# Kernel tuning notes

Hardware: AMD Instinct MI355X
Metric: run time of the kernel (lower is better)

## Reference

```python
import jax, jax.numpy as jnp
import numpy as np

I = 2          # input_features
M = 2          # num_membership_functions
R = M * M      # rules (pairs (m,n) for inputs 0 and 1)
N = 4_194_304  # batch size


def setup_inputs() -> dict:
    key = jax.random.key(0)
    k_x, k_w, k_b = jax.random.split(key, 3)
    x = jax.random.normal(k_x, (I, N), dtype=jnp.float32)
    # generalized-bell MF params from membership_funcs_params [[a,b,c]...]
    a = jnp.ones((I, M), dtype=jnp.float32)                      # widths
    b = jnp.full((I, M), 2.0, dtype=jnp.float32)                 # slopes
    c = jnp.tile(jnp.array([-1.0, 1.0], dtype=jnp.float32), (I, 1))  # centers
    # per-rule first-order Sugeno (TSK) defuzzifier: f_r = W[r] . x + Bd[r]
    W = 0.1 * jax.random.normal(k_w, (R, I), dtype=jnp.float32)
    Bd = 0.1 * jax.random.normal(k_b, (R,), dtype=jnp.float32)
    return {"x": x, "a": a, "b": b, "c": c, "W": W, "Bd": Bd}


def reference(x, a, b, c, W, Bd):
    # Layer 1+2 (fuzzification): generalized bell mu = 1/(1+|(x-c)/a|^(2b))
    # mu: [I, M, N]
    mu = 1.0 / (1.0 + jnp.abs((x[:, None, :] - c[:, :, None]) / a[:, :, None]) ** (2.0 * b[:, :, None]))
    # Layer 3 (rule firing strengths): product over the (i=0,m)x(j=1,n) pairs
    # rule index r = m*M + n, matching the original nested loop order. [R, N]
    rules = (mu[0, :, None, :] * mu[1, None, :, :]).reshape(R, N)
    # Layer 4 (normalization): w_r / sum_r w_r
    norm = rules / jnp.sum(rules, axis=0, keepdims=True)
    # Layer 5 (defuzzification): per-rule linear consequent, weighted
    f = W @ x + Bd[:, None]            # [R, N]
    # Layer 6 (aggregation): sum over rules -> [N]
    return jnp.sum(norm * f, axis=0)
```

## Files before the change

### kernel.cpp

```cpp
#include <hip/hip_runtime.h>


__global__ __launch_bounds__(256) void anfis_kernel(
    const float* __restrict__ x,
    const float* __restrict__ a,
    const float* __restrict__ b,
    const float* __restrict__ c,
    const float* __restrict__ W,
    const float* __restrict__ Bd,
    float* __restrict__ out,
    int N)
{
    float ia[2][2], nca[2][2], tb[2][2];
#pragma unroll
    for (int i = 0; i < 2; ++i) {
#pragma unroll
        for (int m = 0; m < 2; ++m) {
            float av = a[i * 2 + m];
            float bv = b[i * 2 + m];
            float cv = c[i * 2 + m];
            float r  = 1.0f / av;
            ia[i][m]  = r;
            nca[i][m] = -cv * r;
            tb[i][m]  = 2.0f * bv;
        }
    }
    float w0[4], w1[4], bd[4];
#pragma unroll
    for (int r = 0; r < 4; ++r) {
        w0[r] = W[r * 2 + 0];
        w1[r] = W[r * 2 + 1];
        bd[r] = Bd[r];
    }

    int idx = (blockIdx.x * blockDim.x + threadIdx.x) * 4;
    if (idx >= N) return;

    float4 v0 = *reinterpret_cast<const float4*>(x + idx);
    float4 v1 = *reinterpret_cast<const float4*>(x + N + idx);

    float xs0[4] = {v0.x, v0.y, v0.z, v0.w};
    float xs1[4] = {v1.x, v1.y, v1.z, v1.w};
    float res[4];

#pragma unroll
    for (int k = 0; k < 4; ++k) {
        float x0 = xs0[k], x1 = xs1[k];

        float mu0[2], mu1[2];
#pragma unroll
        for (int m = 0; m < 2; ++m) {
            float t = fabsf(fmaf(x0, ia[0][m], nca[0][m]));
            float u = __builtin_amdgcn_exp2f(tb[0][m] * __builtin_amdgcn_logf(t));
            mu0[m] = __builtin_amdgcn_rcpf(1.0f + u);
            float s = fabsf(fmaf(x1, ia[1][m], nca[1][m]));
            float v = __builtin_amdgcn_exp2f(tb[1][m] * __builtin_amdgcn_logf(s));
            mu1[m] = __builtin_amdgcn_rcpf(1.0f + v);
        }

        float den = (mu0[0] + mu0[1]) * (mu1[0] + mu1[1]);

        float num = 0.0f;
#pragma unroll
        for (int m = 0; m < 2; ++m) {
#pragma unroll
            for (int n2 = 0; n2 < 2; ++n2) {
                int r = m * 2 + n2;
                float f = fmaf(w0[r], x0, fmaf(w1[r], x1, bd[r]));
                num = fmaf(mu0[m] * mu1[n2], f, num);
            }
        }
        res[k] = num * __builtin_amdgcn_rcpf(den);
    }

    float4 o = {res[0], res[1], res[2], res[3]};
    *reinterpret_cast<float4*>(out + idx) = o;
}

extern "C" void kernel_launch(void* const* d_in, const int* in_sizes, int n_in,
                              void* d_out, int out_size, void* d_ws, size_t ws_size,
                              hipStream_t stream) {
    const float* x  = (const float*)d_in[0];
    const float* a  = (const float*)d_in[1];
    const float* b  = (const float*)d_in[2];
    const float* c  = (const float*)d_in[3];
    const float* W  = (const float*)d_in[4];
    const float* Bd = (const float*)d_in[5];
    float* out = (float*)d_out;

    int N = out_size;
    int n4 = (N + 3) / 4;
    int block = 256;
    int grid = (n4 + block - 1) / block;

    anfis_kernel<<<grid, block, 0, stream>>>(x, a, b, c, W, Bd, out, N);
}
```

Measured before the change: 16.27 us.

## Specialize bell MF for b=2 with polynomial eval and drop per-MF reciprocals

Rewrites the normalization algebraically, multiplying numerator and denominator by the product of the (1+u) terms. This removes the four reciprocals per element. It adds a runtime-checked fast path for b==2, where |x|^4 is computed by squaring instead of log/exp2; the general path stays as a fallback. It also processes 8 elements per thread with two float4 loads and stores per input. The kernel is largely bandwidth bound, so the ALU savings may only partly show, and the larger per-thread work changes the grid size.

```diff
diff --git a/kernel.cpp b/kernel.cpp
--- a/kernel.cpp
+++ b/kernel.cpp
@@ -12,6 +12,7 @@
     int N)
 {
     float ia[2][2], nca[2][2], tb[2][2];
+    bool all_b2 = true;
 #pragma unroll
     for (int i = 0; i < 2; ++i) {
 #pragma unroll
@@ -23,6 +24,7 @@
             ia[i][m]  = r;
             nca[i][m] = -cv * r;
             tb[i][m]  = 2.0f * bv;
+            all_b2 = all_b2 && (bv == 2.0f);
         }
     }
     float w0[4], w1[4], bd[4];
@@ -33,48 +35,72 @@
         bd[r] = Bd[r];
     }
 
-    int idx = (blockIdx.x * blockDim.x + threadIdx.x) * 4;
+    int idx = (blockIdx.x * blockDim.x + threadIdx.x) * 8;
     if (idx >= N) return;
 
-    float4 v0 = *reinterpret_cast<const float4*>(x + idx);
-    float4 v1 = *reinterpret_cast<const float4*>(x + N + idx);
+    const float4* p0 = reinterpret_cast<const float4*>(x + idx);
+    const float4* p1 = reinterpret_cast<const float4*>(x + N + idx);
+    float4 v0a = p0[0], v0b = p0[1];
+    float4 v1a = p1[0], v1b = p1[1];
 
-    float xs0[4] = {v0.x, v0.y, v0.z, v0.w};
-    float xs1[4] = {v1.x, v1.y, v1.z, v1.w};
-    float res[4];
+    float xs0[8] = {v0a.x, v0a.y, v0a.z, v0a.w, v0b.x, v0b.y, v0b.z, v0b.w};
+    float xs1[8] = {v1a.x, v1a.y, v1a.z, v1a.w, v1b.x, v1b.y, v1b.z, v1b.w};
+    float res[8];
 
+    if (all_b2) {
 #pragma unroll
-    for (int k = 0; k < 4; ++k) {
-        float x0 = xs0[k], x1 = xs1[k];
+        for (int k = 0; k < 8; ++k) {
+            float x0 = xs0[k], x1 = xs1[k];
+            float t00 = fmaf(x0, ia[0][0], nca[0][0]); t00 *= t00;
+            float t01 = fmaf(x0, ia[0][1], nca[0][1]); t01 *= t01;
+            float t10 = fmaf(x1, ia[1][0], nca[1][0]); t10 *= t10;
+            float t11 = fmaf(x1, ia[1][1], nca[1][1]); t11 *= t11;
+            float A0 = fmaf(t00, t00, 1.0f);
+            float A1 = fmaf(t01, t01, 1.0f);
+            float B0 = fmaf(t10, t10, 1.0f);
+            float B1 = fmaf(t11, t11, 1.0f);
 
-        float mu0[2], mu1[2];
+            float den = (A0 + A1) * (B0 + B1);
+
+            float f0 = fmaf(w0[0], x0, fmaf(w1[0], x1, bd[0]));
+            float f1 = fmaf(w0[1], x0, fmaf(w1[1], x1, bd[1]));
+            float f2 = fmaf(w0[2], x0, fmaf(w1[2], x1, bd[2]));
+            float f3 = fmaf(w0[3], x0, fmaf(w1[3], x1, bd[3]));
+            float num = (A1 * B1) * f0;
+            num = fmaf(A1 * B0, f1, num);
+            num = fmaf(A0 * B1, f2, num);
+            num = fmaf(A0 * B0, f3, num);
+
+            res[k] = num * __builtin_amdgcn_rcpf(den);
+        }
+    } else {
 #pragma unroll
-        for (int m = 0; m < 2; ++m) {
-            float t = fabsf(fmaf(x0, ia[0][m], nca[0][m]));
-            float u = __builtin_amdgcn_exp2f(tb[0][m] * __builtin_amdgcn_logf(t));
-            mu0[m] = __builtin_amdgcn_rcpf(1.0f + u);
-            float s = fabsf(fmaf(x1, ia[1][m], nca[1][m]));
-            float v = __builtin_amdgcn_exp2f(tb[1][m] * __builtin_amdgcn_logf(s));
-            mu1[m] = __builtin_amdgcn_rcpf(1.0f + v);
+        for (int k = 0; k < 8; ++k) {
+            float x0 = xs0[k], x1 = xs1[k];
+            float u00 = __builtin_amdgcn_exp2f(tb[0][0] * __builtin_amdgcn_logf(fabsf(fmaf(x0, ia[0][0], nca[0][0]))));
+            float u01 = __builtin_amdgcn_exp2f(tb[0][1] * __builtin_amdgcn_logf(fabsf(fmaf(x0, ia[0][1], nca[0][1]))));
+            float u10 = __builtin_amdgcn_exp2f(tb[1][0] * __builtin_amdgcn_logf(fabsf(fmaf(x1, ia[1][0], nca[1][0]))));
+            float u11 = __builtin_amdgcn_exp2f(tb[1][1] * __builtin_amdgcn_logf(fabsf(fmaf(x1, ia[1][1], nca[1][1]))));
+            float A0 = 1.0f + u00, A1 = 1.0f + u01;
+            float B0 = 1.0f + u10, B1 = 1.0f + u11;
+            float den = (A0 + A1) * (B0 + B1);
+            float f0 = fmaf(w0[0], x0, fmaf(w1[0], x1, bd[0]));
+            float f1 = fmaf(w0[1], x0, fmaf(w1[1], x1, bd[1]));
+            float f2 = fmaf(w0[2], x0, fmaf(w1[2], x1, bd[2]));
+            float f3 = fmaf(w0[3], x0, fmaf(w1[3], x1, bd[3]));
+            float num = (A1 * B1) * f0;
+            num = fmaf(A1 * B0, f1, num);
+            num = fmaf(A0 * B1, f2, num);
+            num = fmaf(A0 * B0, f3, num);
+            res[k] = num * __builtin_amdgcn_rcpf(den);
         }
-
-        float den = (mu0[0] + mu0[1]) * (mu1[0] + mu1[1]);
-
-        float num = 0.0f;
-#pragma unroll
-        for (int m = 0; m < 2; ++m) {
-#pragma unroll
-            for (int n2 = 0; n2 < 2; ++n2) {
-                int r = m * 2 + n2;
-                float f = fmaf(w0[r], x0, fmaf(w1[r], x1, bd[r]));
-                num = fmaf(mu0[m] * mu1[n2], f, num);
-            }
-        }
-        res[k] = num * __builtin_amdgcn_rcpf(den);
     }
 
-    float4 o = {res[0], res[1], res[2], res[3]};
-    *reinterpret_cast<float4*>(out + idx) = o;
+    float4 oA = {res[0], res[1], res[2], res[3]};
+    float4 oB = {res[4], res[5], res[6], res[7]};
+    float4* po = reinterpret_cast<float4*>(out + idx);
+    po[0] = oA;
+    po[1] = oB;
 }
 
 extern "C" void kernel_launch(void* const* d_in, const int* in_sizes, int n_in,
@@ -89,9 +115,9 @@
     float* out = (float*)d_out;
 
     int N = out_size;
-    int n4 = (N + 3) / 4;
+    int n8 = (N + 7) / 8;
     int block = 256;
-    int grid = (n4 + block - 1) / block;
+    int grid = (n8 + block - 1) / block;
 
     anfis_kernel<<<grid, block, 0, stream>>>(x, a, b, c, W, Bd, out, N);
 }
```

Measured after the change: 13.35 us (median of 3 runs). -18.0%, faster.
